# Kernel tuning notes

Hardware: AMD Instinct MI355X
Metric: run time of the kernel (lower is better)

The kernel has to match this reference:

```python
import jax, jax.numpy as jnp
import numpy as np

TEMPERATURE = 0.07
BASE_TEMPERATURE = 0.07
NUM_HEADS = 4


def setup_inputs() -> dict:
    key = jax.random.key(0)
    k1, k2 = jax.random.split(key)
    features = jax.random.normal(k1, (2048, 2, 256), dtype=jnp.float32)
    labels = jax.random.randint(k2, (2048, 10), 0, 2).astype(jnp.float32)
    return {"features": features, "labels": labels}


def reference(features, labels):
    B, V, E = features.shape
    H = NUM_HEADS
    fs = E // H
    N = B * V

    # torch.cat(torch.unbind(features, dim=1), dim=0): view-major stacking
    f = jnp.transpose(features, (1, 0, 2)).reshape(N, H, fs)
    # F.normalize(dim=-1) with eps=1e-12 clamp
    norm = jnp.sqrt(jnp.sum(f * f, axis=-1, keepdims=True))
    f = f / jnp.maximum(norm, 1e-12)

    # per-head pairwise similarities: dot[i, j, h] = <f[i,h], f[j,h]>  (N, N, H)
    dot = jnp.einsum('ihf,jhf->ijh', f, f)
    heads = jnp.argmax(dot, axis=-1)              # (N, N) head chosen per (anchor, positive)
    dotT = dot / TEMPERATURE

    # logits_max is over j for fixed (i, head); detached in the original
    maxh = jax.lax.stop_gradient(jnp.max(dotT, axis=1))   # (N, H)

    # positive mask, tiled across views, self removed
    mask = (labels @ labels.T) > 0                # (B, B) bool
    mask = jnp.tile(mask, (V, V)).astype(f.dtype)  # (N, N)
    logits_mask = 1.0 - jnp.eye(N, dtype=f.dtype)  # (N, N)
    mask = mask * logits_mask

    # masked exp-sum per (anchor, head): S[i,h] = sum_j lm[i,j] * exp(dotT[i,j,h] - maxh[i,h])
    exp_l = jnp.exp(dotT - maxh[:, None, :])       # (N, N, H)
    S = jnp.einsum('ij,ijh->ih', logits_mask, exp_l)  # (N, H)
    logS = jnp.log(S)

    # select per-pair head: log_prob[i,k] = dotT[i,k,h(i,k)] - maxh[i,h(i,k)] - logS[i,h(i,k)]
    dot_sel = jnp.take_along_axis(dotT, heads[..., None], axis=2)[..., 0]  # (N, N)
    max_sel = jnp.take_along_axis(maxh, heads, axis=1)                     # (N, N)
    logS_sel = jnp.take_along_axis(logS, heads, axis=1)                    # (N, N)
    log_prob = dot_sel - max_sel - logS_sel

    mean_log_prob_pos = jnp.sum(mask * log_prob, axis=1) / jnp.sum(mask, axis=1)
    loss = -(TEMPERATURE / BASE_TEMPERATURE) * mean_log_prob_pos

    finite = jnp.isfinite(loss)
    return jnp.sum(jnp.where(finite, loss, 0.0)) / jnp.sum(finite)
```

## Files before the change

kernel.cpp:

```cpp
#include <hip/hip_runtime.h>
#include <math.h>

#define BS    2048
#define NROW  4096
#define EDIM  256
#define INVT  (1.0f/0.07f)

typedef float  float4v __attribute__((ext_vector_type(4)));
typedef short  short8v __attribute__((ext_vector_type(8)));

static __device__ __forceinline__ unsigned short f2bf(float x) {
    unsigned u = __builtin_bit_cast(unsigned, x);
    u += 0x7fffu + ((u >> 16) & 1u);
    return (unsigned short)(u >> 16);
}

static __device__ __forceinline__ void gload_lds16(const void* g, void* l) {
    __builtin_amdgcn_global_load_lds(
        (const __attribute__((address_space(1))) unsigned int*)g,
        (__attribute__((address_space(3))) unsigned int*)l, 16, 0, 0);
}

__global__ void prep_kernel(const float* __restrict__ feat, const float* __restrict__ labels,
                            unsigned short* __restrict__ fnb, unsigned* __restrict__ bits,
                            float* __restrict__ zacc) {
    const int b = blockIdx.x, t = threadIdx.x;
    if (b < NROW) {
        int bb = b & (BS - 1);
        int v = b >> 11;
        float x = feat[(size_t)bb * (2 * EDIM) + (size_t)v * EDIM + t];
        float ss = x * x;
#pragma unroll
        for (int off = 32; off > 0; off >>= 1)
            ss += __shfl_xor(ss, off, 64);
        float nrm = fmaxf(sqrtf(ss), 1e-12f);
        fnb[(size_t)b * EDIM + t] = f2bf(x / nrm);
    } else {
        int g = (b - NROW) * 256 + t;
        unsigned bb = 0;
#pragma unroll
        for (int d = 0; d < 10; ++d)
            bb |= (labels[g * 10 + d] != 0.0f ? 1u : 0u) << d;
        bits[g] = bb;
        for (int k = g; k < NROW * 9 + 3; k += 2048) zacc[k] = 0.0f;
    }
}

__global__ __launch_bounds__(256, 3) void main_kernel(
    const unsigned short* __restrict__ fnb, const unsigned* __restrict__ bits,
    float* __restrict__ S, float* __restrict__ Num, float* __restrict__ Cnt) {

    __shared__ unsigned short shB[64 * 256];

    const int tid  = threadIdx.x;
    const int lane = tid & 63;
    const int wave = tid >> 6;
    const int quad = lane >> 4;
    const int ml   = lane & 15;
    const int xr   = ml & 7;
    const int i0   = blockIdx.x * 64 + wave * 16;
    const int jc0  = blockIdx.y * 256;

    short8v af[4][2];
    {
        const unsigned short* ap = fnb + (size_t)(i0 + ml) * EDIM + quad * 8;
#pragma unroll
        for (int h = 0; h < 4; ++h)
#pragma unroll
            for (int kk = 0; kk < 2; ++kk)
                af[h][kk] = *(const short8v*)(ap + h * 64 + kk * 32);
    }

    unsigned ibr[4];
#pragma unroll
    for (int r = 0; r < 4; ++r)
        ibr[r] = bits[(i0 + quad * 4 + r) & (BS - 1)];

    float    Sp[4][4] = {};
    float    np[4] = {};
    unsigned cpk[4] = {};

    for (int t = 0; t < 4; ++t) {
        const int j0 = jc0 + t * 64;
        __syncthreads();
#pragma unroll
        for (int q = 0; q < 8; ++q) {
            const int G   = tid + 256 * q;
            const int row = G >> 5;
            const int gg  = (G & 31) ^ (row & 7);
            gload_lds16(fnb + (size_t)(j0 + row) * EDIM + gg * 8, shB + G * 8);
        }
        __syncthreads();

        unsigned jbr[4];
#pragma unroll
        for (int js = 0; js < 4; ++js)
            jbr[js] = bits[(j0 + js * 16 + ml) & (BS - 1)];

        float4v dacc[4][4];
#pragma unroll
        for (int js = 0; js < 4; ++js)
#pragma unroll
            for (int h = 0; h < 4; ++h)
                dacc[js][h] = (float4v){0.f, 0.f, 0.f, 0.f};

#pragma unroll
        for (int h = 0; h < 4; ++h)
#pragma unroll
            for (int kk = 0; kk < 2; ++kk) {
                const int gsw = ((h * 8 + kk * 4 + quad) ^ xr) * 8;
#pragma unroll
                for (int js = 0; js < 4; ++js) {
                    short8v bf = *(const short8v*)(shB + (js * 16 + ml) * 256 + gsw);
                    dacc[js][h] = __builtin_amdgcn_mfma_f32_16x16x32_bf16(af[h][kk], bf, dacc[js][h], 0, 0, 0);
                }
            }

#pragma unroll
        for (int r = 0; r < 4; ++r) {
            const int i = i0 + quad * 4 + r;
            const unsigned ibit = ibr[r];
#pragma unroll
            for (int js = 0; js < 4; ++js) {
                const int j = j0 + js * 16 + ml;
                const float d0 = dacc[js][0][r];
                const float d1 = dacc[js][1][r];
                const float d2 = dacc[js][2][r];
                const float d3 = dacc[js][3][r];
                float bd = d0; int bh = 0;
                if (d1 > bd) { bd = d1; bh = 1; }
                if (d2 > bd) { bd = d2; bh = 2; }
                if (d3 > bd) { bd = d3; bh = 3; }
                const bool off = (i != j);
                const float e0 = __expf(fmaf(d0, INVT, -INVT));
                const float e1 = __expf(fmaf(d1, INVT, -INVT));
                const float e2 = __expf(fmaf(d2, INVT, -INVT));
                const float e3 = __expf(fmaf(d3, INVT, -INVT));
                if (off) {
                    Sp[r][0] += e0; Sp[r][1] += e1; Sp[r][2] += e2; Sp[r][3] += e3;
                }
                if (off && (ibit & jbr[js])) {
                    np[r] += bd;
                    cpk[r] += 1u << (bh * 8);
                }
            }
        }
    }

#pragma unroll
    for (int r = 0; r < 4; ++r) {
        const int i = i0 + quad * 4 + r;
        float v[9];
        v[0] = np[r];
#pragma unroll
        for (int h = 0; h < 4; ++h) v[1 + h] = Sp[r][h];
#pragma unroll
        for (int h = 0; h < 4; ++h) v[5 + h] = (float)((cpk[r] >> (8 * h)) & 255u);
#pragma unroll
        for (int k = 0; k < 9; ++k) {
            float x = v[k];
            x += __shfl_xor(x, 1, 64);
            x += __shfl_xor(x, 2, 64);
            x += __shfl_xor(x, 4, 64);
            x += __shfl_xor(x, 8, 64);
            v[k] = x;
        }
        if (ml == 0) {
            atomicAdd(&Num[i], v[0] * INVT);
#pragma unroll
            for (int h = 0; h < 4; ++h) atomicAdd(&S[i * 4 + h], v[1 + h]);
#pragma unroll
            for (int h = 0; h < 4; ++h) atomicAdd(&Cnt[i * 4 + h], v[5 + h]);
        }
    }
}

__global__ void final_kernel(const float* __restrict__ S, const float* __restrict__ Num,
                             const float* __restrict__ Cnt, float* __restrict__ red,
                             unsigned* __restrict__ done, float* __restrict__ out) {
    const int tid = threadIdx.x;
    const int i = blockIdx.x * 256 + tid;
    float c = 0.f;
    float numr = Num[i];
#pragma unroll
    for (int h = 0; h < 4; ++h) {
        float sh = S[i * 4 + h];
        float ch = Cnt[i * 4 + h];
        numr -= ch * (INVT + logf(sh));
        c += ch;
    }
    float ls = 0.f, lc = 0.f;
    if (c > 0.f) { ls = -(numr / c); lc = 1.f; }

    __shared__ float rs[256], rc[256];
    rs[tid] = ls; rc[tid] = lc;
    __syncthreads();
    for (int s = 128; s > 0; s >>= 1) {
        if (tid < s) { rs[tid] += rs[tid + s]; rc[tid] += rc[tid + s]; }
        __syncthreads();
    }
    if (tid == 0) {
        atomicAdd(&red[0], rs[0]);
        atomicAdd(&red[1], rc[0]);
        __threadfence();
        if (atomicAdd(done, 1u) == 15u) {
            float s = atomicAdd(&red[0], 0.0f);
            float cc = atomicAdd(&red[1], 0.0f);
            out[0] = s / cc;
        }
    }
}

extern "C" void kernel_launch(void* const* d_in, const int* in_sizes, int n_in,
                              void* d_out, int out_size, void* d_ws, size_t ws_size,
                              hipStream_t stream) {
    const float* feat = (const float*)d_in[0];
    const float* labels = (const float*)d_in[1];
    float* out = (float*)d_out;

    char* ws = (char*)d_ws;
    unsigned short* fnb = (unsigned short*)ws;
    float* S = (float*)(ws + (size_t)NROW * EDIM * sizeof(unsigned short));
    float* Num = S + NROW * 4;
    float* Cnt = Num + NROW;
    float* red = Cnt + NROW * 4;
    unsigned* done = (unsigned*)(red + 2);
    unsigned* bits = done + 1;

    prep_kernel<<<NROW + 8, 256, 0, stream>>>(feat, labels, fnb, bits, S);
    main_kernel<<<dim3(64, 16), 256, 0, stream>>>(fnb, bits, S, Num, Cnt);
    final_kernel<<<16, 256, 0, stream>>>(S, Num, Cnt, red, done, out);
}
```

Baseline: 116.6 us.

## Fuse final reduction into main kernel and load B tiles directly from global

Removes the LDS staging of the key tile, so each wave reads bf16 fragments for the MFMAs straight from global memory, and shrinks blocks to two waves over wider column ranges. The separate final kernel is folded into the main kernel: a per-row-block counter picks the last arriving block, which computes the per-row losses and the global mean. This aims to save a kernel launch and the LDS/barrier overhead, at the cost of redundant, less coalesced global/L2 traffic for the B operand.

```diff
diff --git a/kernel.cpp b/kernel.cpp
--- a/kernel.cpp
+++ b/kernel.cpp
@@ -15,10 +15,8 @@
     return (unsigned short)(u >> 16);
 }
 
-static __device__ __forceinline__ void gload_lds16(const void* g, void* l) {
-    __builtin_amdgcn_global_load_lds(
-        (const __attribute__((address_space(1))) unsigned int*)g,
-        (__attribute__((address_space(3))) unsigned int*)l, 16, 0, 0);
+static __device__ __forceinline__ float agent_load(const float* p) {
+    return __hip_atomic_load(p, __ATOMIC_RELAXED, __HIP_MEMORY_SCOPE_AGENT);
 }
 
 __global__ void prep_kernel(const float* __restrict__ feat, const float* __restrict__ labels,
@@ -42,24 +40,24 @@
         for (int d = 0; d < 10; ++d)
             bb |= (labels[g * 10 + d] != 0.0f ? 1u : 0u) << d;
         bits[g] = bb;
-        for (int k = g; k < NROW * 9 + 3; k += 2048) zacc[k] = 0.0f;
-    }
-}
-
-__global__ __launch_bounds__(256, 3) void main_kernel(
+        for (int k = g; k < NROW * 9 + 131; k += 2048) zacc[k] = 0.0f;
+    }
+}
+
+__global__ __launch_bounds__(128, 3) void main_kernel(
     const unsigned short* __restrict__ fnb, const unsigned* __restrict__ bits,
-    float* __restrict__ S, float* __restrict__ Num, float* __restrict__ Cnt) {
-
-    __shared__ unsigned short shB[64 * 256];
+    float* __restrict__ S, float* __restrict__ Num, float* __restrict__ Cnt,
+    float* __restrict__ red, unsigned* __restrict__ done,
+    unsigned* __restrict__ cnt_bx, float* __restrict__ out) {
 
     const int tid  = threadIdx.x;
     const int lane = tid & 63;
     const int wave = tid >> 6;
     const int quad = lane >> 4;
     const int ml   = lane & 15;
-    const int xr   = ml & 7;
-    const int i0   = blockIdx.x * 64 + wave * 16;
-    const int jc0  = blockIdx.y * 256;
+    const int bx   = blockIdx.x;
+    const int i0   = bx * 32 + wave * 16;
+    const int jc0  = blockIdx.y * 512;
 
     short8v af[4][2];
     {
@@ -80,17 +78,8 @@
     float    np[4] = {};
     unsigned cpk[4] = {};
 
-    for (int t = 0; t < 4; ++t) {
+    for (int t = 0; t < 8; ++t) {
         const int j0 = jc0 + t * 64;
-        __syncthreads();
-#pragma unroll
-        for (int q = 0; q < 8; ++q) {
-            const int G   = tid + 256 * q;
-            const int row = G >> 5;
-            const int gg  = (G & 31) ^ (row & 7);
-            gload_lds16(fnb + (size_t)(j0 + row) * EDIM + gg * 8, shB + G * 8);
-        }
-        __syncthreads();
 
         unsigned jbr[4];
 #pragma unroll
@@ -108,12 +97,14 @@
         for (int h = 0; h < 4; ++h)
 #pragma unroll
             for (int kk = 0; kk < 2; ++kk) {
-                const int gsw = ((h * 8 + kk * 4 + quad) ^ xr) * 8;
-#pragma unroll
-                for (int js = 0; js < 4; ++js) {
-                    short8v bf = *(const short8v*)(shB + (js * 16 + ml) * 256 + gsw);
-                    dacc[js][h] = __builtin_amdgcn_mfma_f32_16x16x32_bf16(af[h][kk], bf, dacc[js][h], 0, 0, 0);
-                }
+                const int ko = h * 64 + kk * 32 + quad * 8;
+                short8v bf[4];
+#pragma unroll
+                for (int js = 0; js < 4; ++js)
+                    bf[js] = *(const short8v*)(fnb + (size_t)(j0 + js * 16 + ml) * EDIM + ko);
+#pragma unroll
+                for (int js = 0; js < 4; ++js)
+                    dacc[js][h] = __builtin_amdgcn_mfma_f32_16x16x32_bf16(af[h][kk], bf[js], dacc[js][h], 0, 0, 0);
             }
 
 #pragma unroll
@@ -173,40 +164,41 @@
             for (int h = 0; h < 4; ++h) atomicAdd(&Cnt[i * 4 + h], v[5 + h]);
         }
     }
-}
-
-__global__ void final_kernel(const float* __restrict__ S, const float* __restrict__ Num,
-                             const float* __restrict__ Cnt, float* __restrict__ red,
-                             unsigned* __restrict__ done, float* __restrict__ out) {
-    const int tid = threadIdx.x;
-    const int i = blockIdx.x * 256 + tid;
-    float c = 0.f;
-    float numr = Num[i];
-#pragma unroll
-    for (int h = 0; h < 4; ++h) {
-        float sh = S[i * 4 + h];
-        float ch = Cnt[i * 4 + h];
-        numr -= ch * (INVT + logf(sh));
-        c += ch;
-    }
-    float ls = 0.f, lc = 0.f;
-    if (c > 0.f) { ls = -(numr / c); lc = 1.f; }
-
-    __shared__ float rs[256], rc[256];
-    rs[tid] = ls; rc[tid] = lc;
+
+    __shared__ unsigned flag;
+    __threadfence();
     __syncthreads();
-    for (int s = 128; s > 0; s >>= 1) {
-        if (tid < s) { rs[tid] += rs[tid + s]; rc[tid] += rc[tid + s]; }
-        __syncthreads();
-    }
-    if (tid == 0) {
-        atomicAdd(&red[0], rs[0]);
-        atomicAdd(&red[1], rc[0]);
-        __threadfence();
-        if (atomicAdd(done, 1u) == 15u) {
-            float s = atomicAdd(&red[0], 0.0f);
-            float cc = atomicAdd(&red[1], 0.0f);
-            out[0] = s / cc;
+    if (tid == 0) flag = atomicAdd(&cnt_bx[bx], 1u);
+    __syncthreads();
+    if (flag == 7u && tid < 64) {
+        float ls = 0.f, lc = 0.f;
+        if (tid < 32) {
+            const int i = bx * 32 + tid;
+            float c = 0.f;
+            float numr = agent_load(&Num[i]);
+#pragma unroll
+            for (int h = 0; h < 4; ++h) {
+                float sh = agent_load(&S[i * 4 + h]);
+                float ch = agent_load(&Cnt[i * 4 + h]);
+                numr -= ch * (INVT + logf(sh));
+                c += ch;
+            }
+            if (c > 0.f) { ls = -(numr / c); lc = 1.f; }
+        }
+#pragma unroll
+        for (int off = 1; off < 64; off <<= 1) {
+            ls += __shfl_xor(ls, off, 64);
+            lc += __shfl_xor(lc, off, 64);
+        }
+        if (tid == 0) {
+            atomicAdd(&red[0], ls);
+            atomicAdd(&red[1], lc);
+            __threadfence();
+            if (atomicAdd(done, 1u) == 127u) {
+                float s  = atomicAdd(&red[0], 0.0f);
+                float cc = atomicAdd(&red[1], 0.0f);
+                out[0] = s / cc;
+            }
         }
     }
 }
@@ -225,9 +217,9 @@
     float* Cnt = Num + NROW;
     float* red = Cnt + NROW * 4;
     unsigned* done = (unsigned*)(red + 2);
-    unsigned* bits = done + 1;
+    unsigned* cnt_bx = done + 1;
+    unsigned* bits = cnt_bx + 128;
 
     prep_kernel<<<NROW + 8, 256, 0, stream>>>(feat, labels, fnb, bits, S);
-    main_kernel<<<dim3(64, 16), 256, 0, stream>>>(fnb, bits, S, Num, Cnt);
-    final_kernel<<<16, 256, 0, stream>>>(S, Num, Cnt, red, done, out);
-}
+    main_kernel<<<dim3(128, 8), 128, 0, stream>>>(fnb, bits, S, Num, Cnt, red, done, cnt_bx, out);
+}
```

Result: slower. 164.5 us (+41.1%).
